# Performance work log

Hardware: AMD Instinct MI355X
Metric: run time of the kernel (lower is better)

## Reference

```python
import jax, jax.numpy as jnp
import numpy as np

N = 50000      # nodes
E = 600000     # edges
F_IN = 128     # num_features
H = 128        # conv_dim
C = 10         # num_classes


def setup_inputs() -> dict:
    key = jax.random.key(0)
    ks = jax.random.split(key, 16)
    s = 0.05
    return {
        "x": jax.random.normal(ks[0], (N, F_IN), jnp.float32),
        "edge_index": jax.random.randint(ks[1], (2, E), 0, N, dtype=jnp.int32),
        "W1": jax.random.normal(ks[2], (F_IN, H), jnp.float32) * s,
        "b1": jnp.zeros((H,), jnp.float32),
        "W2": jax.random.normal(ks[3], (H, H), jnp.float32) * s,
        "b2": jnp.zeros((H,), jnp.float32),
        "W3": jax.random.normal(ks[4], (H, H), jnp.float32) * s,
        "b3": jnp.zeros((H,), jnp.float32),
        "fw1": jax.random.normal(ks[5], (3 * H, 128), jnp.float32) * s,
        "fb1": jnp.zeros((128,), jnp.float32),
        "fw2": jax.random.normal(ks[6], (128, 64), jnp.float32) * s,
        "fb2": jnp.zeros((64,), jnp.float32),
        "fw3": jax.random.normal(ks[7], (64, C), jnp.float32) * s,
        "fb3": jnp.zeros((C,), jnp.float32),
    }


def reference(x, edge_index, W1, b1, W2, b2, W3, b3, fw1, fb1, fw2, fb2, fw3, fb3):
    n = x.shape[0]
    # GCN normalization with self-loops (improved=False): A_hat = D^-1/2 (A+I) D^-1/2
    loop = jnp.arange(n, dtype=edge_index.dtype)
    src = jnp.concatenate([edge_index[0], loop])   # [E+N]
    tgt = jnp.concatenate([edge_index[1], loop])   # [E+N]
    deg = jax.ops.segment_sum(jnp.ones_like(src, dtype=x.dtype), tgt, num_segments=n)
    dis = jnp.where(deg > 0, jax.lax.rsqrt(jnp.maximum(deg, 1e-12)), 0.0)
    norm = dis[src] * dis[tgt]                     # [E+N]

    def gcn(h, W, b):
        hw = h @ W                                 # [N,H] linear transform first
        msg = norm[:, None] * hw[src]              # gather + edge scale
        return jax.ops.segment_sum(msg, tgt, num_segments=n) + b  # scatter-add

    x1 = jax.nn.relu(gcn(x, W1, b1))
    x2 = jax.nn.relu(gcn(x1, W2, b2))
    x3 = jax.nn.relu(gcn(x2, W3, b3))
    h = jnp.sum(jnp.concatenate([x1, x2, x3], axis=1), axis=0)  # [3H] sum pool
    h = jax.nn.relu(h @ fw1 + fb1)
    h = jax.nn.relu(h @ fw2 + fb2)
    return h @ fw3 + fb3
```

## Files before the change

kernel.cpp:

```cpp
#include <hip/hip_runtime.h>

#define FDIM 128

typedef __attribute__((ext_vector_type(8))) short bf16x8;
typedef __attribute__((ext_vector_type(4))) float f32x4;
typedef __attribute__((ext_vector_type(2))) float f32x2;


__device__ __forceinline__ unsigned int cvt_bf16(float f) {
    unsigned int u = __float_as_uint(f);
    return (u + 0x7fffu + ((u >> 16) & 1u)) >> 16;
}



__global__ void hist_kernel(const int* __restrict__ tgt, int* __restrict__ count, int ne) {
    int e = blockIdx.x * blockDim.x + threadIdx.x;
    if (e < ne) atomicAdd(&count[tgt[e]], 1);
}

__global__ __launch_bounds__(256) void scan1_kernel(const int* __restrict__ count,
                                                    float* __restrict__ dis,
                                                    int* __restrict__ tpre,
                                                    int* __restrict__ bsum, int n) {
    __shared__ int sm[256];
    int tid = threadIdx.x, blk = blockIdx.x;
    int base = blk * 2048 + tid * 8;
    int s = 0;
    #pragma unroll
    for (int q = 0; q < 8; q++) {
        int i = base + q;
        if (i < n) {
            int c = count[i];
            s += c;
            dis[i] = rsqrtf((float)(c + 1));
        }
    }
    sm[tid] = s;
    __syncthreads();
    for (int off = 1; off < 256; off <<= 1) {
        int v = sm[tid];
        int u = (tid >= off) ? sm[tid - off] : 0;
        __syncthreads();
        sm[tid] = v + u;
        __syncthreads();
    }
    tpre[blk * 256 + tid] = (tid == 0) ? 0 : sm[tid - 1];
    if (tid == 255) bsum[blk] = sm[255];
}

__global__ __launch_bounds__(1024) void scan2_kernel(const int* __restrict__ bsum,
                                                     int* __restrict__ bpre,
                                                     int* __restrict__ rowptr,
                                                     float* __restrict__ pool,
                                                     int n, int nb) {
    __shared__ int sm[1024];
    int tid = threadIdx.x;
    if (tid < 384) pool[tid] = 0.f;
    sm[tid] = (tid < nb) ? bsum[tid] : 0;
    __syncthreads();
    for (int off = 1; off < 1024; off <<= 1) {
        int v = sm[tid];
        int u = (tid >= off) ? sm[tid - off] : 0;
        __syncthreads();
        sm[tid] = v + u;
        __syncthreads();
    }
    if (tid < nb) bpre[tid] = (tid == 0) ? 0 : sm[tid - 1];
    if (tid == nb - 1) rowptr[n] = sm[tid];
}

__global__ __launch_bounds__(256) void scan3_kernel(const int* __restrict__ count,
                                                    const int* __restrict__ tpre,
                                                    const int* __restrict__ bpre,
                                                    int* __restrict__ rowptr,
                                                    int* __restrict__ cursor, int n) {
    int tid = threadIdx.x, blk = blockIdx.x;
    int run = bpre[blk] + tpre[blk * 256 + tid];
    int base = blk * 2048 + tid * 8;
    #pragma unroll
    for (int q = 0; q < 8; q++) {
        int i = base + q;
        if (i < n) {
            rowptr[i] = run;
            cursor[i] = run;
            run += count[i];
        }
    }
}

__global__ void fill_kernel(const int* __restrict__ src, const int* __restrict__ tgt,
                            int* __restrict__ cursor, int* __restrict__ csrs, int ne) {
    int e = blockIdx.x * blockDim.x + threadIdx.x;
    if (e < ne) {
        int t = tgt[e];
        int s = src[e];
        int slot = atomicAdd(&cursor[t], 1);
        csrs[slot] = s;
    }
}


__global__ void xprep_kernel(const float* __restrict__ x, unsigned* __restrict__ x16,
                             int* __restrict__ count, int n, int total) {
    int i = blockIdx.x * blockDim.x + threadIdx.x;
    if (i < total) {
        int m = i >> 6, u = i & 63;
        float lo = x[(size_t)m * 128 + u];
        float hi = x[(size_t)m * 128 + u + 64];
        x16[i] = cvt_bf16(lo) | (cvt_bf16(hi) << 16);
        if (i < n) count[i] = 0;
    }
}

__global__ void wprep_kernel(const float* __restrict__ W1, const float* __restrict__ W2,
                             const float* __restrict__ W3,
                             unsigned* __restrict__ B1, unsigned* __restrict__ B2,
                             unsigned* __restrict__ B3,
                             unsigned short* __restrict__ g8, int n) {
    int i = blockIdx.x * blockDim.x + threadIdx.x;
    if (i < 3 * 8192) {
        int w = i >> 13;
        int j = i & 8191;
        const float* W = (w == 0) ? W1 : (w == 1) ? W2 : W3;
        unsigned* B    = (w == 0) ? B1 : (w == 1) ? B2 : B3;
        int nn = j >> 6, u = j & 63;
        float lo = W[(size_t)u * 128 + nn];
        float hi = W[(size_t)(u + 64) * 128 + nn];
        B[j] = cvt_bf16(lo) | (cvt_bf16(hi) << 16);
    } else if (i < 3 * 8192 + 64) {
        g8[(size_t)n * 64 + (i - 3 * 8192)] = 0;
    }
}


__global__ __launch_bounds__(256) void gemm_kernel(const unsigned* __restrict__ A16,
                                                   const unsigned* __restrict__ Bt16,
                                                   const float* __restrict__ dis,
                                                   unsigned short* __restrict__ g8, int n) {
    int tid  = threadIdx.x;
    int wave = tid >> 6, lane = tid & 63;
    int quad = lane >> 4, r16 = lane & 15;
    int m0 = (blockIdx.x * 4 + wave) * 16;
    if (m0 >= n) return;

    f32x4 acc[8] = {};

    #pragma unroll
    for (int ks = 0; ks < 4; ks++) {
        int m = m0 + r16;
        if (m >= n) m = n - 1;
        uint4 av = *(const uint4*)(A16 + (size_t)m * 64 + ks * 16 + quad * 4);
        bf16x8 af = *(bf16x8*)&av;
        #pragma unroll
        for (int t = 0; t < 8; t++) {
            int ncol = t * 16 + r16;
            uint4 bv = *(const uint4*)(Bt16 + (size_t)ncol * 64 + ks * 16 + quad * 4);
            bf16x8 bf = *(bf16x8*)&bv;
            acc[t] = __builtin_amdgcn_mfma_f32_16x16x32_bf16(af, bf, acc[t], 0, 0, 0);
        }
    }

    #pragma unroll
    for (int r = 0; r < 4; r++) {
        int row = m0 + quad * 4 + r;
        if (row < n) {
            float dr = dis[row];
            #pragma unroll
            for (int t = 0; t < 4; t++) {
                int p = __builtin_amdgcn_cvt_pk_fp8_f32(dr * acc[t][r], dr * acc[t + 4][r], 0, false);
                g8[(size_t)row * 64 + t * 16 + r16] = (unsigned short)(p & 0xffff);
            }
        }
    }
}


#define AGG_ACC(v)                                                     \
    { f32x2 p;                                                         \
      p = __builtin_amdgcn_cvt_pk_f32_fp8((int)v.x, 0); f0[0]+=p.x; f1[0]+=p.y; \
      p = __builtin_amdgcn_cvt_pk_f32_fp8((int)v.x, 1); f0[1]+=p.x; f1[1]+=p.y; \
      p = __builtin_amdgcn_cvt_pk_f32_fp8((int)v.y, 0); f0[2]+=p.x; f1[2]+=p.y; \
      p = __builtin_amdgcn_cvt_pk_f32_fp8((int)v.y, 1); f0[3]+=p.x; f1[3]+=p.y; \
      p = __builtin_amdgcn_cvt_pk_f32_fp8((int)v.z, 0); f0[4]+=p.x; f1[4]+=p.y; \
      p = __builtin_amdgcn_cvt_pk_f32_fp8((int)v.z, 1); f0[5]+=p.x; f1[5]+=p.y; \
      p = __builtin_amdgcn_cvt_pk_f32_fp8((int)v.w, 0); f0[6]+=p.x; f1[6]+=p.y; \
      p = __builtin_amdgcn_cvt_pk_f32_fp8((int)v.w, 1); f0[7]+=p.x; f1[7]+=p.y; }

#define AGG_ISSUE(buf, gi)                                             \
    { int e = (gi) * 8 + j;                                            \
      int s = __shfl(ereg, e);                                         \
      if (b + e >= end) s = n;                                         \
      buf = *(const uint4*)(g8 + (size_t)(unsigned)s * 64u + c * 8); }

__global__ __launch_bounds__(512) void agg_kernel(const unsigned short* __restrict__ g8,
                                                  const float* __restrict__ dis,
                                                  const int* __restrict__ rowptr,
                                                  const int* __restrict__ csrs,
                                                  const float* __restrict__ bias,
                                                  unsigned* __restrict__ out16,
                                                  float* __restrict__ pool, int n) {
    __shared__ float lpool[128];
    int tid = threadIdx.x;
    if (tid < 128) lpool[tid] = 0.f;
    __syncthreads();

    int wave = tid >> 6, lane = tid & 63;
    int j = lane >> 3;
    int c = lane & 7;
    int node0 = (blockIdx.x * 8 + wave) * 4;

    float b0[8], b1[8];
    *(float4*)&b0[0] = *(const float4*)(bias + c * 8);
    *(float4*)&b0[4] = *(const float4*)(bias + c * 8 + 4);
    *(float4*)&b1[0] = *(const float4*)(bias + 64 + c * 8);
    *(float4*)&b1[4] = *(const float4*)(bias + 64 + c * 8 + 4);

    int rpv = 0; float dv = 0.f;
    if (lane <= 4) rpv = rowptr[min(node0 + lane, n)];
    if (lane < 4)  dv  = dis[min(node0 + lane, n - 1)];

    int er[4];
    #pragma unroll
    for (int i = 0; i < 4; i++) {
        int beg = __shfl(rpv, i);
        er[i] = csrs[beg + lane];
    }

    float pp0[8] = {}, pp1[8] = {};

    #pragma unroll
    for (int i = 0; i < 4; i++) {
        int node = node0 + i;
        if (node >= n) break;
        int beg = __shfl(rpv, i);
        int end = __shfl(rpv, i + 1);
        float di = __shfl(dv, i);

        float f0[8] = {}, f1[8] = {};
        {
            int s = (j == 0) ? node : n;
            uint4 sv = *(const uint4*)(g8 + (size_t)(unsigned)s * 64u + c * 8);
            AGG_ACC(sv)
        }
        int ereg = er[i];
        for (int b = beg; b < end; b += 64) {
            if (b != beg) ereg = csrs[b + lane];
            int m = min(64, end - b);
            int ng = (m + 7) >> 3;
            uint4 gv0, gv1;
            AGG_ISSUE(gv0, 0)
            int gi = 0;
            while (true) {
                if (gi + 1 < ng) AGG_ISSUE(gv1, gi + 1)
                AGG_ACC(gv0)
                gi++;
                if (gi >= ng) break;
                if (gi + 1 < ng) AGG_ISSUE(gv0, gi + 1)
                AGG_ACC(gv1)
                gi++;
                if (gi >= ng) break;
            }
        }

        #pragma unroll
        for (int k = 0; k < 8; k++) {
            f0[k] += __shfl_xor(f0[k], 8);  f1[k] += __shfl_xor(f1[k], 8);
            f0[k] += __shfl_xor(f0[k], 16); f1[k] += __shfl_xor(f1[k], 16);
            f0[k] += __shfl_xor(f0[k], 32); f1[k] += __shfl_xor(f1[k], 32);
        }

        float r0[8], r1[8];
        #pragma unroll
        for (int k = 0; k < 8; k++) {
            r0[k] = fmaxf(di * f0[k] + b0[k], 0.f);
            r1[k] = fmaxf(di * f1[k] + b1[k], 0.f);
            pp0[k] += r0[k];
            pp1[k] += r1[k];
        }
        if (out16 && j == 0) {
            uint4 wa, wb;
            wa.x = cvt_bf16(r0[0]) | (cvt_bf16(r1[0]) << 16);
            wa.y = cvt_bf16(r0[1]) | (cvt_bf16(r1[1]) << 16);
            wa.z = cvt_bf16(r0[2]) | (cvt_bf16(r1[2]) << 16);
            wa.w = cvt_bf16(r0[3]) | (cvt_bf16(r1[3]) << 16);
            wb.x = cvt_bf16(r0[4]) | (cvt_bf16(r1[4]) << 16);
            wb.y = cvt_bf16(r0[5]) | (cvt_bf16(r1[5]) << 16);
            wb.z = cvt_bf16(r0[6]) | (cvt_bf16(r1[6]) << 16);
            wb.w = cvt_bf16(r0[7]) | (cvt_bf16(r1[7]) << 16);
            *(uint4*)(out16 + (size_t)node * 64 + c * 8)     = wa;
            *(uint4*)(out16 + (size_t)node * 64 + c * 8 + 4) = wb;
        }
    }

    if (j == 0) {
        #pragma unroll
        for (int k = 0; k < 8; k++) {
            atomicAdd(&lpool[c * 8 + k],      pp0[k]);
            atomicAdd(&lpool[64 + c * 8 + k], pp1[k]);
        }
    }
    __syncthreads();
    if (tid < 128) atomicAdd(&pool[tid], lpool[tid]);
}


__global__ __launch_bounds__(128) void mlp_kernel(const float* __restrict__ pool,
                                                  const float* __restrict__ fw1, const float* __restrict__ fb1,
                                                  const float* __restrict__ fw2, const float* __restrict__ fb2,
                                                  const float* __restrict__ fw3, const float* __restrict__ fb3,
                                                  float* __restrict__ out) {
    __shared__ float h0[384];
    __shared__ float h1[128];
    __shared__ float h2[64];
    int tid = threadIdx.x;
    for (int i = tid; i < 384; i += 128) h0[i] = pool[i];
    __syncthreads();
    {
        float s = fb1[tid];
        for (int k = 0; k < 384; k++) s += h0[k] * fw1[k * 128 + tid];
        h1[tid] = fmaxf(s, 0.f);
    }
    __syncthreads();
    if (tid < 64) {
        float s = fb2[tid];
        for (int k = 0; k < 128; k++) s += h1[k] * fw2[k * 64 + tid];
        h2[tid] = fmaxf(s, 0.f);
    }
    __syncthreads();
    if (tid < 10) {
        float s = fb3[tid];
        for (int k = 0; k < 64; k++) s += h2[k] * fw3[k * 10 + tid];
        out[tid] = s;
    }
}


extern "C" void kernel_launch(void* const* d_in, const int* in_sizes, int n_in,
                              void* d_out, int out_size, void* d_ws, size_t ws_size,
                              hipStream_t stream) {
    const float* x   = (const float*)d_in[0];
    const int*   ei  = (const int*)d_in[1];
    const float* W1  = (const float*)d_in[2];
    const float* b1  = (const float*)d_in[3];
    const float* W2  = (const float*)d_in[4];
    const float* b2  = (const float*)d_in[5];
    const float* W3  = (const float*)d_in[6];
    const float* b3  = (const float*)d_in[7];
    const float* fw1 = (const float*)d_in[8];
    const float* fb1 = (const float*)d_in[9];
    const float* fw2 = (const float*)d_in[10];
    const float* fb2 = (const float*)d_in[11];
    const float* fw3 = (const float*)d_in[12];
    const float* fb3 = (const float*)d_in[13];
    float* out = (float*)d_out;

    const int n  = in_sizes[0] / FDIM;
    const int ne = in_sizes[1] / 2;
    const int* src = ei;
    const int* tgt = ei + ne;

    char* ws = (char*)d_ws;
    size_t packBytes = (size_t)n * 64 * sizeof(unsigned);
    unsigned* x16  = (unsigned*)ws;  ws += packBytes;
    unsigned* A2   = (unsigned*)ws;  ws += packBytes;
    unsigned* A3   = (unsigned*)ws;  ws += packBytes;
    unsigned short* g8 = (unsigned short*)ws; ws += (((size_t)(n + 1) * 64 * 2 + 127) / 128) * 128;
    unsigned* B1t  = (unsigned*)ws;  ws += 128 * 64 * 4;
    unsigned* B2t  = (unsigned*)ws;  ws += 128 * 64 * 4;
    unsigned* B3t  = (unsigned*)ws;  ws += 128 * 64 * 4;
    float* dis  = (float*)ws;        ws += (size_t)n * 4;
    int* count  = (int*)ws;          ws += (size_t)n * 4;
    int* rowptr = (int*)ws;          ws += ((size_t)(n + 4) * 4 / 16) * 16;
    int* cursor = (int*)ws;          ws += (size_t)n * 4;
    int* csrs   = (int*)ws;          ws += (size_t)(ne + 64) * 4;
    float* pool = (float*)ws;        ws += 384 * 4;
    int nb = (n + 2047) / 2048;
    int* tpre = (int*)ws;            ws += (size_t)nb * 256 * 4;
    int* bsum = (int*)ws;            ws += ((size_t)(nb + 3) / 4) * 16;
    int* bpre = (int*)ws;            ws += ((size_t)(nb + 3) / 4) * 16;

    xprep_kernel<<<(n * 64 + 255) / 256, 256, 0, stream>>>(x, x16, count, n, n * 64);
    wprep_kernel<<<(3 * 8192 + 64 + 255) / 256, 256, 0, stream>>>(W1, W2, W3, B1t, B2t, B3t, g8, n);

    hist_kernel<<<(ne + 255) / 256, 256, 0, stream>>>(tgt, count, ne);
    scan1_kernel<<<nb, 256, 0, stream>>>(count, dis, tpre, bsum, n);
    scan2_kernel<<<1, 1024, 0, stream>>>(bsum, bpre, rowptr, pool, n, nb);
    scan3_kernel<<<nb, 256, 0, stream>>>(count, tpre, bpre, rowptr, cursor, n);
    fill_kernel<<<(ne + 255) / 256, 256, 0, stream>>>(src, tgt, cursor, csrs, ne);

    int gemmGrid = (n + 63) / 64;
    int aggGrid  = (n + 31) / 32;

    gemm_kernel<<<gemmGrid, 256, 0, stream>>>(x16, B1t, dis, g8, n);
    agg_kernel<<<aggGrid, 512, 0, stream>>>(g8, dis, rowptr, csrs, b1, A2, pool + 0, n);

    gemm_kernel<<<gemmGrid, 256, 0, stream>>>(A2, B2t, dis, g8, n);
    agg_kernel<<<aggGrid, 512, 0, stream>>>(g8, dis, rowptr, csrs, b2, A3, pool + 128, n);

    gemm_kernel<<<gemmGrid, 256, 0, stream>>>(A3, B3t, dis, g8, n);
    agg_kernel<<<aggGrid, 512, 0, stream>>>(g8, dis, rowptr, csrs, b3, (unsigned*)nullptr, pool + 256, n);

    mlp_kernel<<<1, 128, 0, stream>>>(pool, fw1, fb1, fw2, fb2, fw3, fb3, out);
}
```

Measured before the change: 455.2 us.

## Software-pipeline neighbor gathers across nodes in aggregation and merge prep kernels

Restructures the aggregation kernel so the first 32 neighbor rows and the self-loop row of the next node are loaded before the current node's reduction and epilogue run. Neighbors are now fetched in rounds of four outstanding loads instead of a double buffer, which aims to hide gather latency across node boundaries. The x and weight conversion kernels are also merged into one launch to save a kernel launch. The change costs more registers for the prefetch buffers, which may lower occupancy.

```diff
diff --git a/kernel.cpp b/kernel.cpp
--- a/kernel.cpp
+++ b/kernel.cpp
@@ -101,35 +101,36 @@
 }
 
 
-__global__ void xprep_kernel(const float* __restrict__ x, unsigned* __restrict__ x16,
-                             int* __restrict__ count, int n, int total) {
+__global__ void prep_kernel(const float* __restrict__ x,
+                            const float* __restrict__ W1, const float* __restrict__ W2,
+                            const float* __restrict__ W3,
+                            unsigned* __restrict__ x16,
+                            unsigned* __restrict__ B1, unsigned* __restrict__ B2,
+                            unsigned* __restrict__ B3,
+                            unsigned short* __restrict__ g8,
+                            int* __restrict__ count, int n) {
     int i = blockIdx.x * blockDim.x + threadIdx.x;
-    if (i < total) {
+    int nx = n * 64;
+    if (i < nx) {
         int m = i >> 6, u = i & 63;
         float lo = x[(size_t)m * 128 + u];
         float hi = x[(size_t)m * 128 + u + 64];
         x16[i] = cvt_bf16(lo) | (cvt_bf16(hi) << 16);
         if (i < n) count[i] = 0;
-    }
-}
-
-__global__ void wprep_kernel(const float* __restrict__ W1, const float* __restrict__ W2,
-                             const float* __restrict__ W3,
-                             unsigned* __restrict__ B1, unsigned* __restrict__ B2,
-                             unsigned* __restrict__ B3,
-                             unsigned short* __restrict__ g8, int n) {
-    int i = blockIdx.x * blockDim.x + threadIdx.x;
-    if (i < 3 * 8192) {
-        int w = i >> 13;
-        int j = i & 8191;
-        const float* W = (w == 0) ? W1 : (w == 1) ? W2 : W3;
-        unsigned* B    = (w == 0) ? B1 : (w == 1) ? B2 : B3;
-        int nn = j >> 6, u = j & 63;
-        float lo = W[(size_t)u * 128 + nn];
-        float hi = W[(size_t)(u + 64) * 128 + nn];
-        B[j] = cvt_bf16(lo) | (cvt_bf16(hi) << 16);
-    } else if (i < 3 * 8192 + 64) {
-        g8[(size_t)n * 64 + (i - 3 * 8192)] = 0;
+    } else {
+        int k = i - nx;
+        if (k < 3 * 8192) {
+            int w = k >> 13;
+            int jj = k & 8191;
+            const float* W = (w == 0) ? W1 : (w == 1) ? W2 : W3;
+            unsigned* B    = (w == 0) ? B1 : (w == 1) ? B2 : B3;
+            int nn = jj >> 6, u = jj & 63;
+            float lo = W[(size_t)u * 128 + nn];
+            float hi = W[(size_t)(u + 64) * 128 + nn];
+            B[jj] = cvt_bf16(lo) | (cvt_bf16(hi) << 16);
+        } else if (k < 3 * 8192 + 64) {
+            g8[(size_t)n * 64 + (k - 3 * 8192)] = 0;
+        }
     }
 }
 
@@ -187,11 +188,22 @@
       p = __builtin_amdgcn_cvt_pk_f32_fp8((int)v.w, 0); f0[6]+=p.x; f1[6]+=p.y; \
       p = __builtin_amdgcn_cvt_pk_f32_fp8((int)v.w, 1); f0[7]+=p.x; f1[7]+=p.y; }
 
-#define AGG_ISSUE(buf, gi)                                             \
-    { int e = (gi) * 8 + j;                                            \
+#define ISSUE1(buf, ereg, EBASE, mlim)                                 \
+    { int e = (EBASE) + j;                                             \
       int s = __shfl(ereg, e);                                         \
-      if (b + e >= end) s = n;                                         \
+      if (e >= (mlim)) s = n;                                          \
       buf = *(const uint4*)(g8 + (size_t)(unsigned)s * 64u + c * 8); }
+
+#define ROUND4(ereg, Q0, mlim)                                         \
+    { uint4 u0, u1, u2, u3;                                            \
+      ISSUE1(u0, ereg, (Q0) + 0, mlim)                                 \
+      if ((mlim) > (Q0) + 8)  ISSUE1(u1, ereg, (Q0) + 8,  mlim)        \
+      if ((mlim) > (Q0) + 16) ISSUE1(u2, ereg, (Q0) + 16, mlim)        \
+      if ((mlim) > (Q0) + 24) ISSUE1(u3, ereg, (Q0) + 24, mlim)        \
+      AGG_ACC(u0)                                                      \
+      if ((mlim) > (Q0) + 8)  AGG_ACC(u1)                              \
+      if ((mlim) > (Q0) + 16) AGG_ACC(u2)                              \
+      if ((mlim) > (Q0) + 24) AGG_ACC(u3) }
 
 __global__ __launch_bounds__(512) void agg_kernel(const unsigned short* __restrict__ g8,
                                                   const float* __restrict__ dis,
@@ -227,40 +239,57 @@
         er[i] = csrs[beg + lane];
     }
 
+    uint4 c0, c1, c2, c3, sB;
+    {
+        int deg = __shfl(rpv, 1) - __shfl(rpv, 0);
+        int mlim = min(deg, 64);
+        int ereg = er[0];
+        ISSUE1(c0, ereg, 0, mlim)
+        if (deg > 8)  ISSUE1(c1, ereg, 8,  mlim)
+        if (deg > 16) ISSUE1(c2, ereg, 16, mlim)
+        if (deg > 24) ISSUE1(c3, ereg, 24, mlim)
+        int s = (node0 < n && j == 0) ? node0 : n;
+        sB = *(const uint4*)(g8 + (size_t)(unsigned)s * 64u + c * 8);
+    }
+
     float pp0[8] = {}, pp1[8] = {};
 
     #pragma unroll
     for (int i = 0; i < 4; i++) {
         int node = node0 + i;
-        if (node >= n) break;
+        bool ok = node < n;
         int beg = __shfl(rpv, i);
         int end = __shfl(rpv, i + 1);
+        int deg = end - beg;
         float di = __shfl(dv, i);
 
         float f0[8] = {}, f1[8] = {};
-        {
-            int s = (j == 0) ? node : n;
-            uint4 sv = *(const uint4*)(g8 + (size_t)(unsigned)s * 64u + c * 8);
-            AGG_ACC(sv)
-        }
-        int ereg = er[i];
-        for (int b = beg; b < end; b += 64) {
-            if (b != beg) ereg = csrs[b + lane];
-            int m = min(64, end - b);
-            int ng = (m + 7) >> 3;
-            uint4 gv0, gv1;
-            AGG_ISSUE(gv0, 0)
-            int gi = 0;
-            while (true) {
-                if (gi + 1 < ng) AGG_ISSUE(gv1, gi + 1)
-                AGG_ACC(gv0)
-                gi++;
-                if (gi >= ng) break;
-                if (gi + 1 < ng) AGG_ISSUE(gv0, gi + 1)
-                AGG_ACC(gv1)
-                gi++;
-                if (gi >= ng) break;
+        AGG_ACC(c0)
+        if (deg > 8)  AGG_ACC(c1)
+        if (deg > 16) AGG_ACC(c2)
+        if (deg > 24) AGG_ACC(c3)
+        if (deg > 32) {
+            int mlim = min(deg, 64);
+            ROUND4(er[i], 32, mlim)
+            for (int b2 = 64; b2 < deg; b2 += 64) {
+                int ereg2 = csrs[beg + b2 + lane];
+                int ml2 = min(deg - b2, 64);
+                ROUND4(ereg2, 0, ml2)
+                if (ml2 > 32) ROUND4(ereg2, 32, ml2)
             }
+        }
+
+        uint4 n0v, n1v, n2v, n3v, nS;
+        if (i < 3) {
+            int nd = __shfl(rpv, i + 2) - end;
+            int nml = min(nd, 64);
+            int ner = er[i + 1];
+            ISSUE1(n0v, ner, 0, nml)
+            if (nd > 8)  ISSUE1(n1v, ner, 8,  nml)
+            if (nd > 16) ISSUE1(n2v, ner, 16, nml)
+            if (nd > 24) ISSUE1(n3v, ner, 24, nml)
+            int s = (node + 1 < n && j == 0) ? (node + 1) : n;
+            nS = *(const uint4*)(g8 + (size_t)(unsigned)s * 64u + c * 8);
         }
 
         #pragma unroll
@@ -269,28 +298,33 @@
             f0[k] += __shfl_xor(f0[k], 16); f1[k] += __shfl_xor(f1[k], 16);
             f0[k] += __shfl_xor(f0[k], 32); f1[k] += __shfl_xor(f1[k], 32);
         }
-
-        float r0[8], r1[8];
-        #pragma unroll
-        for (int k = 0; k < 8; k++) {
-            r0[k] = fmaxf(di * f0[k] + b0[k], 0.f);
-            r1[k] = fmaxf(di * f1[k] + b1[k], 0.f);
-            pp0[k] += r0[k];
-            pp1[k] += r1[k];
-        }
-        if (out16 && j == 0) {
-            uint4 wa, wb;
-            wa.x = cvt_bf16(r0[0]) | (cvt_bf16(r1[0]) << 16);
-            wa.y = cvt_bf16(r0[1]) | (cvt_bf16(r1[1]) << 16);
-            wa.z = cvt_bf16(r0[2]) | (cvt_bf16(r1[2]) << 16);
-            wa.w = cvt_bf16(r0[3]) | (cvt_bf16(r1[3]) << 16);
-            wb.x = cvt_bf16(r0[4]) | (cvt_bf16(r1[4]) << 16);
-            wb.y = cvt_bf16(r0[5]) | (cvt_bf16(r1[5]) << 16);
-            wb.z = cvt_bf16(r0[6]) | (cvt_bf16(r1[6]) << 16);
-            wb.w = cvt_bf16(r0[7]) | (cvt_bf16(r1[7]) << 16);
-            *(uint4*)(out16 + (size_t)node * 64 + c * 8)     = wa;
-            *(uint4*)(out16 + (size_t)node * 64 + c * 8 + 4) = wb;
-        }
+        if (j == 0) AGG_ACC(sB)
+
+        if (ok) {
+            float r0[8], r1[8];
+            #pragma unroll
+            for (int k = 0; k < 8; k++) {
+                r0[k] = fmaxf(di * f0[k] + b0[k], 0.f);
+                r1[k] = fmaxf(di * f1[k] + b1[k], 0.f);
+                pp0[k] += r0[k];
+                pp1[k] += r1[k];
+            }
+            if (out16 && j == 0) {
+                uint4 wa, wb;
+                wa.x = cvt_bf16(r0[0]) | (cvt_bf16(r1[0]) << 16);
+                wa.y = cvt_bf16(r0[1]) | (cvt_bf16(r1[1]) << 16);
+                wa.z = cvt_bf16(r0[2]) | (cvt_bf16(r1[2]) << 16);
+                wa.w = cvt_bf16(r0[3]) | (cvt_bf16(r1[3]) << 16);
+                wb.x = cvt_bf16(r0[4]) | (cvt_bf16(r1[4]) << 16);
+                wb.y = cvt_bf16(r0[5]) | (cvt_bf16(r1[5]) << 16);
+                wb.z = cvt_bf16(r0[6]) | (cvt_bf16(r1[6]) << 16);
+                wb.w = cvt_bf16(r0[7]) | (cvt_bf16(r1[7]) << 16);
+                *(uint4*)(out16 + (size_t)node * 64 + c * 8)     = wa;
+                *(uint4*)(out16 + (size_t)node * 64 + c * 8 + 4) = wb;
+            }
+        }
+
+        c0 = n0v; c1 = n1v; c2 = n2v; c3 = n3v; sB = nS;
     }
 
     if (j == 0) {
@@ -380,8 +414,8 @@
     int* bsum = (int*)ws;            ws += ((size_t)(nb + 3) / 4) * 16;
     int* bpre = (int*)ws;            ws += ((size_t)(nb + 3) / 4) * 16;
 
-    xprep_kernel<<<(n * 64 + 255) / 256, 256, 0, stream>>>(x, x16, count, n, n * 64);
-    wprep_kernel<<<(3 * 8192 + 64 + 255) / 256, 256, 0, stream>>>(W1, W2, W3, B1t, B2t, B3t, g8, n);
+    int prepTotal = n * 64 + 3 * 8192 + 64;
+    prep_kernel<<<(prepTotal + 255) / 256, 256, 0, stream>>>(x, W1, W2, W3, x16, B1t, B2t, B3t, g8, count, n);
 
     hist_kernel<<<(ne + 255) / 256, 256, 0, stream>>>(tgt, count, ne);
     scan1_kernel<<<nb, 256, 0, stream>>>(count, dis, tpre, bsum, n);
```

Measured after the change: 462.8 us. About the same (+1.7%).
